# Performance work log

Measured on AMD Instinct MI355X. Metric: run time of the kernel, lower is better.

The kernel has to match this reference:

```python
import jax, jax.numpy as jnp
import numpy as np

V, D, NL, S, B = 32000, 1024, 2, 2048, 1
EXPAND, N, K = 2, 16, 4
DI = EXPAND * D
EPS = 1e-5


def setup_inputs() -> dict:
    key = jax.random.key(0)
    ks = jax.random.split(key, 10)
    std = 0.02
    inp = {
        "input_ids": jax.random.randint(ks[0], (B, S), 0, V),
        "embedding": jax.random.normal(ks[1], (V, D), jnp.float32) * std,
        "in_proj_w": jax.random.normal(ks[2], (NL, 2 * DI, D), jnp.float32) * std,
        "conv_w": jax.random.normal(ks[3], (NL, DI, 1, K), jnp.float32) * std,
        "conv_b": jnp.zeros((NL, DI), jnp.float32),
        "x_proj_w": jax.random.normal(ks[4], (NL, 2 * N, DI), jnp.float32) * std,
        "dt_proj_w": jax.random.normal(ks[5], (NL, DI, DI), jnp.float32) * std,
        "dt_proj_b": jnp.zeros((NL, DI), jnp.float32),
        "A_log": jnp.broadcast_to(jnp.log(jnp.arange(1, N + 1, dtype=jnp.float32)), (NL, DI, N)).copy(),
        "D_param": jnp.ones((NL, DI), jnp.float32),
        "out_proj_w": jax.random.normal(ks[6], (NL, D, DI), jnp.float32) * std,
        "norm_w": jnp.ones((NL, D), jnp.float32),
        "norm_f_w": jnp.ones((D,), jnp.float32),
        "lm_head_w": jax.random.normal(ks[7], (V, D), jnp.float32) * std,
    }
    return inp


def rmsnorm(x, w):
    rms = jnp.sqrt(jnp.mean(x * x, axis=-1, keepdims=True) + EPS)
    return x / rms * w


def silu(x):
    return x * jax.nn.sigmoid(x)


def ssm_layer(x, in_w, cw, cb, xp_w, dt_w, dt_b, A_log, Dp):
    b, s, _ = x.shape
    xz = jnp.einsum("bsd,ed->bse", x, in_w)  # (B,S,2*DI)
    xi, z = jnp.split(xz, 2, axis=-1)
    # depthwise causal conv1d
    xc = jnp.swapaxes(xi, 1, 2)  # (B,DI,S)
    xc = jax.lax.conv_general_dilated(
        xc, cw, window_strides=(1,), padding=[(K - 1, 0)],
        dimension_numbers=("NCH", "OIH", "NCH"), feature_group_count=DI,
    ) + cb[None, :, None]
    xi = silu(jnp.swapaxes(xc, 1, 2))  # (B,S,DI)
    bc = jnp.einsum("bsd,ed->bse", xi, xp_w)  # (B,S,2N)
    Bc, Cc = jnp.split(bc, 2, axis=-1)
    dt = jax.nn.softplus(jnp.einsum("bsd,ed->bse", xi, dt_w) + dt_b)
    A = -jnp.exp(A_log)  # (DI,N)
    dA = jnp.exp(dt[..., None] * A)                      # (B,S,DI,N)
    dBu = dt[..., None] * Bc[:, :, None, :] * xi[..., None]  # (B,S,DI,N)

    def step(h, t):
        dA_t, dBu_t, C_t, u_t = t
        h = dA_t * h + dBu_t                     # (B,DI,N)
        y = jnp.sum(h * C_t[:, None, :], axis=-1) + Dp * u_t  # (B,DI)
        return h, y

    xs = (jnp.swapaxes(dA, 0, 1), jnp.swapaxes(dBu, 0, 1),
          jnp.swapaxes(Cc, 0, 1), jnp.swapaxes(xi, 0, 1))
    h0 = jnp.zeros((b, DI, N), x.dtype)
    _, ys = jax.lax.scan(step, h0, xs)
    y = jnp.swapaxes(ys, 0, 1)  # (B,S,DI)
    y = y * silu(z)
    return y


def reference(input_ids, embedding, in_proj_w, conv_w, conv_b, x_proj_w,
              dt_proj_w, dt_proj_b, A_log, D_param, out_proj_w, norm_w,
              norm_f_w, lm_head_w):
    x = embedding[input_ids]  # (B,S,D)
    for l in range(NL):
        h = rmsnorm(x, norm_w[l])
        y = ssm_layer(h, in_proj_w[l], conv_w[l], conv_b[l], x_proj_w[l],
                      dt_proj_w[l], dt_proj_b[l], A_log[l], D_param[l])
        x = x + jnp.einsum("bse,de->bsd", y, out_proj_w[l])
    x = rmsnorm(x, norm_f_w)
    logits = jnp.einsum("bsd,vd->bsv", x, lm_head_w)
    return logits
```

## Files before the change

kernel.cpp:

```cpp
#include <hip/hip_runtime.h>
#include <hip/hip_bf16.h>
#include <stdint.h>
#include <stddef.h>

#define Vv   32000
#define Dd   1024
#define NLay 2
#define Ss   2048
#define Nn   16
#define Kc   4
#define DIc  2048
#define EPSf 1e-5f
#define LCH  32
#define NCHc (Ss / LCH)
#define CATR 2176

typedef __attribute__((ext_vector_type(8))) short bf16x8;
typedef __attribute__((ext_vector_type(4))) float f32x4;

__device__ __forceinline__ short f2bf(float f) {
  union { float f; unsigned u; } a; a.f = f;
  return (short)((a.u + 0x7FFFu + ((a.u >> 16) & 1u)) >> 16);
}
__device__ __forceinline__ float bf2f(short s) {
  union { unsigned u; float f; } a; a.u = ((unsigned)(unsigned short)s) << 16;
  return a.f;
}
__device__ __forceinline__ int hswz(int r) { return (r & 3) ^ ((r >> 2) & 3); }

struct CvtSeg { const float* s; short* d; unsigned n4; };
struct CvtBatch { CvtSeg seg[7]; unsigned tot4; };
__global__ __launch_bounds__(256) void cvt_all_k(CvtBatch b) {
  for (unsigned idx = blockIdx.x * 256 + threadIdx.x; idx < b.tot4;
       idx += gridDim.x * 256) {
    unsigned r = idx;
    int sg = 0;
    while (sg < 6 && r >= b.seg[sg].n4) { r -= b.seg[sg].n4; ++sg; }
    float4 v = ((const float4*)b.seg[sg].s)[r];
    short4 o;
    o.x = f2bf(v.x); o.y = f2bf(v.y); o.z = f2bf(v.z); o.w = f2bf(v.w);
    ((short4*)b.seg[sg].d)[r] = o;
  }
}

__global__ __launch_bounds__(256) void embed_norm_k(const int* __restrict__ ids,
                                                    const float* __restrict__ emb,
                                                    const float* __restrict__ w,
                                                    float* __restrict__ x,
                                                    short* __restrict__ o) {
  int s = blockIdx.x, t = threadIdx.x;
  int id = ids[s];
  float4 v = ((const float4*)(emb + (size_t)id * Dd))[t];
  ((float4*)(x + (size_t)s * Dd))[t] = v;
  float ss = v.x * v.x + v.y * v.y + v.z * v.z + v.w * v.w;
#pragma unroll
  for (int off = 32; off; off >>= 1) ss += __shfl_down(ss, off);
  __shared__ float red[4];
  if ((t & 63) == 0) red[t >> 6] = ss;
  __syncthreads();
  ss = red[0] + red[1] + red[2] + red[3];
  float rinv = rsqrtf(ss * (1.0f / Dd) + EPSf);
  float4 wv = ((const float4*)w)[t];
  short4 ov;
  ov.x = f2bf(v.x * rinv * wv.x);
  ov.y = f2bf(v.y * rinv * wv.y);
  ov.z = f2bf(v.z * rinv * wv.z);
  ov.w = f2bf(v.w * rinv * wv.w);
  ((short4*)(o + (size_t)s * Dd))[t] = ov;
}

__global__ __launch_bounds__(256) void rmsnorm_k(const float* __restrict__ x,
                                                 const float* __restrict__ w,
                                                 short* __restrict__ o) {
  int s = blockIdx.x, t = threadIdx.x;
  float4 v = ((const float4*)(x + (size_t)s * Dd))[t];
  float ss = v.x * v.x + v.y * v.y + v.z * v.z + v.w * v.w;
#pragma unroll
  for (int off = 32; off; off >>= 1) ss += __shfl_down(ss, off);
  __shared__ float red[4];
  if ((t & 63) == 0) red[t >> 6] = ss;
  __syncthreads();
  ss = red[0] + red[1] + red[2] + red[3];
  float rinv = rsqrtf(ss * (1.0f / Dd) + EPSf);
  float4 wv = ((const float4*)w)[t];
  short4 ov;
  ov.x = f2bf(v.x * rinv * wv.x);
  ov.y = f2bf(v.y * rinv * wv.y);
  ov.z = f2bf(v.z * rinv * wv.z);
  ov.w = f2bf(v.w * rinv * wv.w);
  ((short4*)(o + (size_t)s * Dd))[t] = ov;
}

template <int BM, int BN, int WM, int WN, bool RESID, bool CAT>
__global__ __launch_bounds__(WM * WN * 64, 2) void gemm_ring(
    const short* __restrict__ A, const short* __restrict__ B,
    float* C, const float* resb, float* C2, int M, int N, int K, int nMt) {
  constexpr int NT = WM * WN * 64;
  constexpr int FM = BM / (WM * 16);
  constexpr int FN = BN / (WN * 16);
  constexpr int PA = BM * 4 / NT;
  constexpr int PB = BN * 4 / NT;
  static_assert(PA + PB == 4, "vmcnt literals assume 4 loads per stage");
  __shared__ short lds[4][(BM + BN) * 32];
  const int t = threadIdx.x;
  const int lane = t & 63;
  const int w = t >> 6;
  const int wm = w / WN, wn = w % WN;
  const int lr = lane & 15, l4 = lane >> 4;
  const int nwg = gridDim.x;
  const int chunk = nwg >> 3;
  const int wg = (blockIdx.x & 7) * chunk + (blockIdx.x >> 3);
  const int mi = wg % nMt, ni = wg / nMt;
  const size_t rowBase = (size_t)mi * BM, colBase = (size_t)ni * BN;

  const short* aSrc[PA]; int aOff[PA];
  const short* bSrc[PB]; int bOff[PB];
#pragma unroll
  for (int p = 0; p < PA; ++p) {
    int q = p * NT + t;
    int row = q >> 2, s = q & 3;
    aSrc[p] = A + (rowBase + row) * K + ((s ^ hswz(row)) << 3);
    aOff[p] = q * 8;
  }
#pragma unroll
  for (int p = 0; p < PB; ++p) {
    int q = p * NT + t;
    int row = q >> 2, s = q & 3;
    bSrc[p] = B + (colBase + row) * K + ((s ^ hswz(row)) << 3);
    bOff[p] = BM * 32 + q * 8;
  }
  auto stage = [&](int buf, int k0) {
#pragma unroll
    for (int p = 0; p < PA; ++p)
      __builtin_amdgcn_global_load_lds(
          (__attribute__((address_space(1))) unsigned int*)(aSrc[p] + k0),
          (__attribute__((address_space(3))) unsigned int*)(&lds[buf][aOff[p]]), 16, 0, 0);
#pragma unroll
    for (int p = 0; p < PB; ++p)
      __builtin_amdgcn_global_load_lds(
          (__attribute__((address_space(1))) unsigned int*)(bSrc[p] + k0),
          (__attribute__((address_space(3))) unsigned int*)(&lds[buf][bOff[p]]), 16, 0, 0);
  };

  f32x4 acc[FM][FN];
#pragma unroll
  for (int i = 0; i < FM; i++)
#pragma unroll
    for (int j = 0; j < FN; j++) acc[i][j] = f32x4{0.f, 0.f, 0.f, 0.f};

  const int KT = K >> 5;
  stage(0, 0); stage(1, 32); stage(2, 64);
  for (int kt = 0; kt < KT; ++kt) {
    const int rem = KT - 1 - kt;
    __builtin_amdgcn_sched_barrier(0);
    if (rem >= 2)      asm volatile("s_waitcnt vmcnt(8)" ::: "memory");
    else if (rem == 1) asm volatile("s_waitcnt vmcnt(4)" ::: "memory");
    else               asm volatile("s_waitcnt vmcnt(0)" ::: "memory");
    __builtin_amdgcn_sched_barrier(0);
    __builtin_amdgcn_s_barrier();
    __builtin_amdgcn_sched_barrier(0);
    if (kt + 3 < KT) stage((kt + 3) & 3, (kt + 3) << 5);
    const short* la = &lds[kt & 3][0];
    const short* lb = &lds[kt & 3][BM * 32];
    bf16x8 av[FM], bv[FN];
#pragma unroll
    for (int i = 0; i < FM; i++) {
      int r = wm * (FM * 16) + i * 16 + lr;
      av[i] = *(const bf16x8*)&la[r * 32 + ((l4 ^ hswz(r)) << 3)];
    }
#pragma unroll
    for (int j = 0; j < FN; j++) {
      int r = wn * (FN * 16) + j * 16 + lr;
      bv[j] = *(const bf16x8*)&lb[r * 32 + ((l4 ^ hswz(r)) << 3)];
    }
    __builtin_amdgcn_s_setprio(1);
#pragma unroll
    for (int i = 0; i < FM; i++)
#pragma unroll
      for (int j = 0; j < FN; j++)
        acc[i][j] = __builtin_amdgcn_mfma_f32_16x16x32_bf16(av[i], bv[j], acc[i][j], 0, 0, 0);
    __builtin_amdgcn_s_setprio(0);
  }
#pragma unroll
  for (int i = 0; i < FM; i++) {
#pragma unroll
    for (int j = 0; j < FN; j++) {
      size_t r0 = rowBase + wm * (FM * 16) + i * 16 + l4 * 4;
      size_t c = colBase + wn * (FN * 16) + j * 16 + lr;
#pragma unroll
      for (int rr = 0; rr < 4; rr++) {
        size_t r = r0 + rr;
        float v = acc[i][j][rr];
        if (CAT) {
          if (c < DIc) {
            float xv = v + resb[c];
            C[r * DIc + c] = fmaxf(xv, 0.f) + log1pf(__expf(-fabsf(xv)));
          } else if (c < DIc + 2 * Nn) {
            C2[r * (2 * Nn) + (c - DIc)] = v;
          }
        } else {
          size_t idx = r * N + c;
          if (RESID) v += resb[idx];
          C[idx] = v;
        }
      }
    }
  }
}

__global__ __launch_bounds__(512, 2) void gemm256(const short* __restrict__ A,
                                                  const short* __restrict__ B,
                                                  float* __restrict__ C,
                                                  int M, int N, int K, int nMt) {
  __shared__ short lds[2][2][256 * 64];
  const int t = threadIdx.x;
  const int lane = t & 63;
  const int w = t >> 6;
  const int wm = w >> 2, wn = w & 3;
  const int lr = lane & 15, l4 = lane >> 4;
  const int nwg = gridDim.x;
  const int chunk = nwg >> 3;
  const int wg = (blockIdx.x & 7) * chunk + (blockIdx.x >> 3);
  const int mi = wg % nMt, ni = wg / nMt;
  const size_t rowBase = (size_t)mi * 256, colBase = (size_t)ni * 256;

  const short* aSrc[4]; const short* bSrc[4];
  int ldsOff[4];
#pragma unroll
  for (int p = 0; p < 4; ++p) {
    int q = p * 512 + t;
    int row = q >> 3, s = q & 7;
    int ks = (s ^ (row & 7)) * 8;
    aSrc[p] = A + (rowBase + row) * K + ks;
    bSrc[p] = B + (colBase + row) * K + ks;
    ldsOff[p] = q * 8;
  }
  auto stage = [&](int buf, int k0) {
#pragma unroll
    for (int p = 0; p < 4; ++p)
      __builtin_amdgcn_global_load_lds(
          (__attribute__((address_space(1))) unsigned int*)(aSrc[p] + k0),
          (__attribute__((address_space(3))) unsigned int*)(&lds[buf][0][ldsOff[p]]), 16, 0, 0);
#pragma unroll
    for (int p = 0; p < 4; ++p)
      __builtin_amdgcn_global_load_lds(
          (__attribute__((address_space(1))) unsigned int*)(bSrc[p] + k0),
          (__attribute__((address_space(3))) unsigned int*)(&lds[buf][1][ldsOff[p]]), 16, 0, 0);
  };

  f32x4 acc[8][4];
#pragma unroll
  for (int i = 0; i < 8; i++)
#pragma unroll
    for (int j = 0; j < 4; j++) acc[i][j] = f32x4{0.f, 0.f, 0.f, 0.f};

  stage(0, 0);
  const int KT = K >> 6;
  for (int kt = 0; kt < KT; ++kt) {
    const int cur = kt & 1;
    __syncthreads();
    bf16x8 a0[4][2], b0[4][2];
#pragma unroll
    for (int i = 0; i < 4; i++)
#pragma unroll
      for (int kq = 0; kq < 2; kq++) {
        int r = wm * 128 + i * 16 + lr;
        int ks = kq * 4 + l4;
        a0[i][kq] = *(const bf16x8*)&lds[cur][0][r * 64 + ((ks ^ (r & 7)) << 3)];
      }
#pragma unroll
    for (int j = 0; j < 4; j++)
#pragma unroll
      for (int kq = 0; kq < 2; kq++) {
        int r = wn * 64 + j * 16 + lr;
        int ks = kq * 4 + l4;
        b0[j][kq] = *(const bf16x8*)&lds[cur][1][r * 64 + ((ks ^ (r & 7)) << 3)];
      }
    if (kt + 1 < KT) stage(cur ^ 1, (kt + 1) << 6);
    __builtin_amdgcn_s_setprio(1);
#pragma unroll
    for (int i = 0; i < 4; i++)
#pragma unroll
      for (int j = 0; j < 4; j++)
#pragma unroll
        for (int kq = 0; kq < 2; kq++)
          acc[i][j] = __builtin_amdgcn_mfma_f32_16x16x32_bf16(a0[i][kq], b0[j][kq], acc[i][j], 0, 0, 0);
    __builtin_amdgcn_s_setprio(0);
    bf16x8 a1[4][2];
#pragma unroll
    for (int i = 0; i < 4; i++)
#pragma unroll
      for (int kq = 0; kq < 2; kq++) {
        int r = wm * 128 + 64 + i * 16 + lr;
        int ks = kq * 4 + l4;
        a1[i][kq] = *(const bf16x8*)&lds[cur][0][r * 64 + ((ks ^ (r & 7)) << 3)];
      }
    __builtin_amdgcn_s_setprio(1);
#pragma unroll
    for (int i = 0; i < 4; i++)
#pragma unroll
      for (int j = 0; j < 4; j++)
#pragma unroll
        for (int kq = 0; kq < 2; kq++)
          acc[i + 4][j] = __builtin_amdgcn_mfma_f32_16x16x32_bf16(a1[i][kq], b0[j][kq], acc[i + 4][j], 0, 0, 0);
    __builtin_amdgcn_s_setprio(0);
  }
#pragma unroll
  for (int i = 0; i < 8; i++) {
#pragma unroll
    for (int j = 0; j < 4; j++) {
      size_t r0 = rowBase + wm * 128 + i * 16 + l4 * 4;
      size_t c = colBase + wn * 64 + j * 16 + lr;
#pragma unroll
      for (int rr = 0; rr < 4; rr++)
        C[(r0 + rr) * N + c] = acc[i][j][rr];
    }
  }
}

__global__ __launch_bounds__(256) void conv_silu_k(const float* __restrict__ xz,
                                                   const float* __restrict__ cw,
                                                   const float* __restrict__ cb,
                                                   short* __restrict__ xiC) {
  int idx = blockIdx.x * 256 + threadIdx.x;
  int s = idx / (DIc / 4), c4 = idx - s * (DIc / 4);
  const float4* xz4 = (const float4*)xz;
  const size_t rstride = 2 * DIc / 4;
  float4 zero = {0.f, 0.f, 0.f, 0.f};
  float4 x0 = (s >= 3) ? xz4[(size_t)(s - 3) * rstride + c4] : zero;
  float4 x1 = (s >= 2) ? xz4[(size_t)(s - 2) * rstride + c4] : zero;
  float4 x2 = (s >= 1) ? xz4[(size_t)(s - 1) * rstride + c4] : zero;
  float4 x3 = xz4[(size_t)s * rstride + c4];
  float4 cbv = ((const float4*)cb)[c4];
  short4 ov;
  float xs[4][4] = {{x0.x, x1.x, x2.x, x3.x}, {x0.y, x1.y, x2.y, x3.y},
                    {x0.z, x1.z, x2.z, x3.z}, {x0.w, x1.w, x2.w, x3.w}};
  float cbs[4] = {cbv.x, cbv.y, cbv.z, cbv.w};
  short os[4];
#pragma unroll
  for (int j = 0; j < 4; j++) {
    float4 wv = ((const float4*)cw)[c4 * 4 + j];
    float acc = cbs[j] + wv.x * xs[j][0] + wv.y * xs[j][1] + wv.z * xs[j][2] + wv.w * xs[j][3];
    os[j] = f2bf(acc / (1.f + __expf(-acc)));
  }
  ov.x = os[0]; ov.y = os[1]; ov.z = os[2]; ov.w = os[3];
  ((short4*)xiC)[idx] = ov;
}

__global__ __launch_bounds__(256) void scan_pass1(const float* __restrict__ dt,
                                                  const short* __restrict__ u,
                                                  const float* __restrict__ bc,
                                                  const float* __restrict__ alog,
                                                  float* __restrict__ Ap,
                                                  float* __restrict__ Hl) {
  const int j = blockIdx.x;
  const int d = blockIdx.y * 256 + threadIdx.x;
  __shared__ float sB[LCH][Nn];
  for (int q = threadIdx.x; q < LCH * Nn; q += 256) {
    int tt = q >> 4, n = q & 15;
    sB[tt][n] = bc[(size_t)(j * LCH + tt) * 32 + n];
  }
  __syncthreads();
  float Ar[Nn], h[Nn], ap[Nn];
#pragma unroll
  for (int n = 0; n < Nn; n++) {
    Ar[n] = -__expf(alog[d * Nn + n]); h[n] = 0.f; ap[n] = 1.f;
  }
  const int t0 = j * LCH;
  for (int tt = 0; tt < LCH; tt++) {
    size_t gi = (size_t)(t0 + tt) * DIc + d;
    float dtv = dt[gi];
    float uv = bf2f(u[gi]);
    float dtu = dtv * uv;
#pragma unroll
    for (int n = 0; n < Nn; n++) {
      float a = __expf(dtv * Ar[n]);
      h[n] = a * h[n] + dtu * sB[tt][n];
      ap[n] *= a;
    }
  }
  size_t base = ((size_t)j * DIc + d) * Nn;
#pragma unroll
  for (int n = 0; n < Nn; n++) { Ap[base + n] = ap[n]; Hl[base + n] = h[n]; }
}

__global__ __launch_bounds__(256) void scan_combine(const float* __restrict__ Ap,
                                                    const float* __restrict__ Hl,
                                                    float* __restrict__ Hi) {
  int idx = blockIdx.x * 256 + threadIdx.x;
  float h = 0.f;
  for (int j = 0; j < NCHc; j++) {
    size_t o = (size_t)j * DIc * Nn + idx;
    Hi[o] = h;
    h = Ap[o] * h + Hl[o];
  }
}

__global__ __launch_bounds__(256) void scan_pass2(const float* __restrict__ dt,
                                                  const short* __restrict__ u,
                                                  const float* __restrict__ bc,
                                                  const float* __restrict__ alog,
                                                  const float* __restrict__ Hinit,
                                                  const float* __restrict__ Dp,
                                                  const float* __restrict__ xz,
                                                  short* __restrict__ y) {
  const int j = blockIdx.x;
  const int d = blockIdx.y * 256 + threadIdx.x;
  __shared__ float sB[LCH][Nn], sC[LCH][Nn];
  for (int q = threadIdx.x; q < LCH * Nn; q += 256) {
    int tt = q >> 4, n = q & 15;
    size_t r = (size_t)(j * LCH + tt) * 32;
    sB[tt][n] = bc[r + n];
    sC[tt][n] = bc[r + 16 + n];
  }
  __syncthreads();
  float Ar[Nn], h[Nn];
  size_t hb = ((size_t)j * DIc + d) * Nn;
#pragma unroll
  for (int n = 0; n < Nn; n++) {
    Ar[n] = -__expf(alog[d * Nn + n]); h[n] = Hinit[hb + n];
  }
  float dp = Dp[d];
  const int t0 = j * LCH;
  for (int tt = 0; tt < LCH; tt++) {
    size_t gi = (size_t)(t0 + tt) * DIc + d;
    float dtv = dt[gi];
    float uv = bf2f(u[gi]);
    float dtu = dtv * uv;
    float yv = dp * uv;
#pragma unroll
    for (int n = 0; n < Nn; n++) {
      float a = __expf(dtv * Ar[n]);
      h[n] = a * h[n] + dtu * sB[tt][n];
      yv += h[n] * sC[tt][n];
    }
    float zv = xz[(size_t)(t0 + tt) * (2 * DIc) + DIc + d];
    float sz = zv / (1.f + __expf(-zv));
    y[gi] = f2bf(yv * sz);
  }
}

extern "C" void kernel_launch(void* const* d_in, const int* in_sizes, int n_in,
                              void* d_out, int out_size, void* d_ws, size_t ws_size,
                              hipStream_t stream) {
  (void)in_sizes; (void)n_in; (void)out_size; (void)ws_size;
  const int* ids = (const int*)d_in[0];
  const float* emb = (const float*)d_in[1];
  const float* in_proj_w = (const float*)d_in[2];
  const float* conv_w = (const float*)d_in[3];
  const float* conv_b = (const float*)d_in[4];
  const float* x_proj_w = (const float*)d_in[5];
  const float* dt_proj_w = (const float*)d_in[6];
  const float* dt_proj_b = (const float*)d_in[7];
  const float* A_log = (const float*)d_in[8];
  const float* D_param = (const float*)d_in[9];
  const float* out_proj_w = (const float*)d_in[10];
  const float* norm_w = (const float*)d_in[11];
  const float* norm_f_w = (const float*)d_in[12];
  const float* lm_head_w = (const float*)d_in[13];
  float* logits = (float*)d_out;

  char* ws = (char*)d_ws;
  size_t woff = 0;
  auto walloc = [&](size_t bytes) { void* p = ws + woff; woff += (bytes + 255) & ~(size_t)255; return p; };
  float* x     = (float*)walloc((size_t)Ss * Dd * 4);
  short* xfbf  = (short*)walloc((size_t)Ss * Dd * 2);
  short* w_lm  = (short*)walloc((size_t)Vv * Dd * 2);

  char* sc = (char*)d_out;
  size_t soff = 0;
  auto salloc = [&](size_t bytes) { void* p = sc + soff; soff += (bytes + 255) & ~(size_t)255; return p; };
  float* xz   = (float*)salloc((size_t)Ss * 2 * DIc * 4);
  float* dtb  = (float*)salloc((size_t)Ss * DIc * 4);
  float* bc   = (float*)salloc((size_t)Ss * 32 * 4);
  float* Ap   = (float*)salloc((size_t)NCHc * DIc * Nn * 4);
  float* Hl   = (float*)salloc((size_t)NCHc * DIc * Nn * 4);
  float* Hi   = (float*)salloc((size_t)NCHc * DIc * Nn * 4);
  short* hbf  = (short*)salloc((size_t)Ss * Dd * 2);
  short* xiC  = (short*)salloc((size_t)Ss * DIc * 2);
  short* ybf  = (short*)salloc((size_t)Ss * DIc * 2);
  short* w_in = (short*)salloc((size_t)NLay * 2 * DIc * Dd * 2);
  short* w_cat= (short*)salloc((size_t)NLay * CATR * DIc * 2);
  short* w_out= (short*)salloc((size_t)NLay * Dd * DIc * 2);

  CvtBatch cb2{};
  unsigned tot = 0;
  auto addseg = [&](int i, const float* s, short* d, size_t n) {
    cb2.seg[i].s = s; cb2.seg[i].d = d; cb2.seg[i].n4 = (unsigned)(n / 4);
    tot += (unsigned)(n / 4);
  };
  addseg(0, in_proj_w, w_in, (size_t)NLay * 2 * DIc * Dd);
  addseg(1, out_proj_w, w_out, (size_t)NLay * Dd * DIc);
  addseg(2, lm_head_w, w_lm, (size_t)Vv * Dd);
  addseg(3, dt_proj_w, w_cat, (size_t)DIc * DIc);
  addseg(4, x_proj_w, w_cat + (size_t)DIc * DIc, (size_t)2 * Nn * DIc);
  addseg(5, dt_proj_w + (size_t)DIc * DIc, w_cat + (size_t)CATR * DIc, (size_t)DIc * DIc);
  addseg(6, x_proj_w + (size_t)2 * Nn * DIc,
         w_cat + (size_t)CATR * DIc + (size_t)DIc * DIc, (size_t)2 * Nn * DIc);
  cb2.tot4 = tot;
  cvt_all_k<<<dim3(4096), dim3(256), 0, stream>>>(cb2);

  embed_norm_k<<<dim3(Ss), dim3(256), 0, stream>>>(ids, emb, norm_w, x, hbf);

  for (int l = 0; l < NLay; l++) {
    if (l > 0)
      rmsnorm_k<<<dim3(Ss), dim3(256), 0, stream>>>(x, norm_w + (size_t)l * Dd, hbf);
    gemm_ring<128, 128, 2, 2, false, false><<<dim3(512), dim3(256), 0, stream>>>(
        hbf, w_in + (size_t)l * 2 * DIc * Dd, xz, nullptr, nullptr, Ss, 2 * DIc, Dd, 16);
    conv_silu_k<<<dim3(Ss * DIc / 4 / 256), dim3(256), 0, stream>>>(
        xz, conv_w + (size_t)l * DIc * Kc, conv_b + (size_t)l * DIc, xiC);
    gemm_ring<128, 128, 2, 2, false, true><<<dim3(272), dim3(256), 0, stream>>>(
        xiC, w_cat + (size_t)l * CATR * DIc, dtb, dt_proj_b + (size_t)l * DIc, bc,
        Ss, CATR, DIc, 16);
    scan_pass1<<<dim3(NCHc, DIc / 256), dim3(256), 0, stream>>>(
        dtb, xiC, bc, A_log + (size_t)l * DIc * Nn, Ap, Hl);
    scan_combine<<<dim3(DIc * Nn / 256), dim3(256), 0, stream>>>(Ap, Hl, Hi);
    scan_pass2<<<dim3(NCHc, DIc / 256), dim3(256), 0, stream>>>(
        dtb, xiC, bc, A_log + (size_t)l * DIc * Nn, Hi,
        D_param + (size_t)l * DIc, xz, ybf);
    gemm_ring<128, 128, 2, 2, true, false><<<dim3(128), dim3(256), 0, stream>>>(
        ybf, w_out + (size_t)l * Dd * DIc, x, x, nullptr, Ss, Dd, DIc, 16);
  }

  rmsnorm_k<<<dim3(Ss), dim3(256), 0, stream>>>(x, norm_f_w, xfbf);
  gemm256<<<dim3(1000), dim3(512), 0, stream>>>(xfbf, w_lm, logits, Ss, Vv, Dd, 8);
}
```

Baseline: 644.1 us.

## Store in_proj output as bf16, add nontemporal stores, batch scan_combine loads

The in_proj GEMM now writes its xz output as bf16 instead of fp32, and the conv and scan_pass2 kernels read the bf16 values, halving that intermediate's traffic. The weight-conversion kernel and the final logits GEMM use nontemporal stores to avoid polluting cache. scan_combine loads eight chunk entries before running its serial recurrence, which exposes memory-level parallelism. Rounding xz (including z) to bf16 adds some precision loss.

```diff
diff --git a/kernel.cpp b/kernel.cpp
--- a/kernel.cpp
+++ b/kernel.cpp
@@ -16,6 +16,7 @@
 #define CATR 2176
 
 typedef __attribute__((ext_vector_type(8))) short bf16x8;
+typedef __attribute__((ext_vector_type(4))) short s16x4;
 typedef __attribute__((ext_vector_type(4))) float f32x4;
 
 __device__ __forceinline__ short f2bf(float f) {
@@ -37,9 +38,9 @@
     int sg = 0;
     while (sg < 6 && r >= b.seg[sg].n4) { r -= b.seg[sg].n4; ++sg; }
     float4 v = ((const float4*)b.seg[sg].s)[r];
-    short4 o;
+    s16x4 o;
     o.x = f2bf(v.x); o.y = f2bf(v.y); o.z = f2bf(v.z); o.w = f2bf(v.w);
-    ((short4*)b.seg[sg].d)[r] = o;
+    __builtin_nontemporal_store(o, &((s16x4*)b.seg[sg].d)[r]);
   }
 }
 
@@ -91,7 +92,7 @@
   ((short4*)(o + (size_t)s * Dd))[t] = ov;
 }
 
-template <int BM, int BN, int WM, int WN, bool RESID, bool CAT>
+template <int BM, int BN, int WM, int WN, bool RESID, bool CAT, bool OBF16 = false>
 __global__ __launch_bounds__(WM * WN * 64, 2) void gemm_ring(
     const short* __restrict__ A, const short* __restrict__ B,
     float* C, const float* resb, float* C2, int M, int N, int K, int nMt) {
@@ -198,6 +199,8 @@
           } else if (c < DIc + 2 * Nn) {
             C2[r * (2 * Nn) + (c - DIc)] = v;
           }
+        } else if (OBF16) {
+          ((short*)C)[r * N + c] = f2bf(v);
         } else {
           size_t idx = r * N + c;
           if (RESID) v += resb[idx];
@@ -313,28 +316,29 @@
       size_t c = colBase + wn * 64 + j * 16 + lr;
 #pragma unroll
       for (int rr = 0; rr < 4; rr++)
-        C[(r0 + rr) * N + c] = acc[i][j][rr];
-    }
-  }
-}
-
-__global__ __launch_bounds__(256) void conv_silu_k(const float* __restrict__ xz,
+        __builtin_nontemporal_store(acc[i][j][rr], &C[(r0 + rr) * N + c]);
+    }
+  }
+}
+
+__global__ __launch_bounds__(256) void conv_silu_k(const short* __restrict__ xz,
                                                    const float* __restrict__ cw,
                                                    const float* __restrict__ cb,
                                                    short* __restrict__ xiC) {
   int idx = blockIdx.x * 256 + threadIdx.x;
   int s = idx / (DIc / 4), c4 = idx - s * (DIc / 4);
-  const float4* xz4 = (const float4*)xz;
+  const short4* xz4 = (const short4*)xz;
   const size_t rstride = 2 * DIc / 4;
-  float4 zero = {0.f, 0.f, 0.f, 0.f};
-  float4 x0 = (s >= 3) ? xz4[(size_t)(s - 3) * rstride + c4] : zero;
-  float4 x1 = (s >= 2) ? xz4[(size_t)(s - 2) * rstride + c4] : zero;
-  float4 x2 = (s >= 1) ? xz4[(size_t)(s - 1) * rstride + c4] : zero;
-  float4 x3 = xz4[(size_t)s * rstride + c4];
+  short4 zero = {0, 0, 0, 0};
+  short4 x0 = (s >= 3) ? xz4[(size_t)(s - 3) * rstride + c4] : zero;
+  short4 x1 = (s >= 2) ? xz4[(size_t)(s - 2) * rstride + c4] : zero;
+  short4 x2 = (s >= 1) ? xz4[(size_t)(s - 1) * rstride + c4] : zero;
+  short4 x3 = xz4[(size_t)s * rstride + c4];
   float4 cbv = ((const float4*)cb)[c4];
-  short4 ov;
-  float xs[4][4] = {{x0.x, x1.x, x2.x, x3.x}, {x0.y, x1.y, x2.y, x3.y},
-                    {x0.z, x1.z, x2.z, x3.z}, {x0.w, x1.w, x2.w, x3.w}};
+  float xs[4][4] = {{bf2f(x0.x), bf2f(x1.x), bf2f(x2.x), bf2f(x3.x)},
+                    {bf2f(x0.y), bf2f(x1.y), bf2f(x2.y), bf2f(x3.y)},
+                    {bf2f(x0.z), bf2f(x1.z), bf2f(x2.z), bf2f(x3.z)},
+                    {bf2f(x0.w), bf2f(x1.w), bf2f(x2.w), bf2f(x3.w)}};
   float cbs[4] = {cbv.x, cbv.y, cbv.z, cbv.w};
   short os[4];
 #pragma unroll
@@ -343,6 +347,7 @@
     float acc = cbs[j] + wv.x * xs[j][0] + wv.y * xs[j][1] + wv.z * xs[j][2] + wv.w * xs[j][3];
     os[j] = f2bf(acc / (1.f + __expf(-acc)));
   }
+  short4 ov;
   ov.x = os[0]; ov.y = os[1]; ov.z = os[2]; ov.w = os[3];
   ((short4*)xiC)[idx] = ov;
 }
@@ -389,10 +394,19 @@
                                                     float* __restrict__ Hi) {
   int idx = blockIdx.x * 256 + threadIdx.x;
   float h = 0.f;
-  for (int j = 0; j < NCHc; j++) {
-    size_t o = (size_t)j * DIc * Nn + idx;
-    Hi[o] = h;
-    h = Ap[o] * h + Hl[o];
+  for (int j0 = 0; j0 < NCHc; j0 += 8) {
+    float ap[8], hl[8];
+#pragma unroll
+    for (int u = 0; u < 8; ++u) {
+      size_t o = (size_t)(j0 + u) * DIc * Nn + idx;
+      ap[u] = Ap[o]; hl[u] = Hl[o];
+    }
+#pragma unroll
+    for (int u = 0; u < 8; ++u) {
+      size_t o = (size_t)(j0 + u) * DIc * Nn + idx;
+      Hi[o] = h;
+      h = ap[u] * h + hl[u];
+    }
   }
 }
 
@@ -402,7 +416,7 @@
                                                   const float* __restrict__ alog,
                                                   const float* __restrict__ Hinit,
                                                   const float* __restrict__ Dp,
-                                                  const float* __restrict__ xz,
+                                                  const short* __restrict__ xz,
                                                   short* __restrict__ y) {
   const int j = blockIdx.x;
   const int d = blockIdx.y * 256 + threadIdx.x;
@@ -434,7 +448,7 @@
       h[n] = a * h[n] + dtu * sB[tt][n];
       yv += h[n] * sC[tt][n];
     }
-    float zv = xz[(size_t)(t0 + tt) * (2 * DIc) + DIc + d];
+    float zv = bf2f(xz[(size_t)(t0 + tt) * (2 * DIc) + DIc + d]);
     float sz = zv / (1.f + __expf(-zv));
     y[gi] = f2bf(yv * sz);
   }
@@ -470,7 +484,7 @@
   char* sc = (char*)d_out;
   size_t soff = 0;
   auto salloc = [&](size_t bytes) { void* p = sc + soff; soff += (bytes + 255) & ~(size_t)255; return p; };
-  float* xz   = (float*)salloc((size_t)Ss * 2 * DIc * 4);
+  short* xz   = (short*)salloc((size_t)Ss * 2 * DIc * 2);
   float* dtb  = (float*)salloc((size_t)Ss * DIc * 4);
   float* bc   = (float*)salloc((size_t)Ss * 32 * 4);
   float* Ap   = (float*)salloc((size_t)NCHc * DIc * Nn * 4);
@@ -505,8 +519,8 @@
   for (int l = 0; l < NLay; l++) {
     if (l > 0)
       rmsnorm_k<<<dim3(Ss), dim3(256), 0, stream>>>(x, norm_w + (size_t)l * Dd, hbf);
-    gemm_ring<128, 128, 2, 2, false, false><<<dim3(512), dim3(256), 0, stream>>>(
-        hbf, w_in + (size_t)l * 2 * DIc * Dd, xz, nullptr, nullptr, Ss, 2 * DIc, Dd, 16);
+    gemm_ring<128, 128, 2, 2, false, false, true><<<dim3(512), dim3(256), 0, stream>>>(
+        hbf, w_in + (size_t)l * 2 * DIc * Dd, (float*)xz, nullptr, nullptr, Ss, 2 * DIc, Dd, 16);
     conv_silu_k<<<dim3(Ss * DIc / 4 / 256), dim3(256), 0, stream>>>(
         xz, conv_w + (size_t)l * DIc * Kc, conv_b + (size_t)l * DIc, xiC);
     gemm_ring<128, 128, 2, 2, false, true><<<dim3(272), dim3(256), 0, stream>>>(
```

New measurement: 653.3 us. No clear change (+1.4%).
